# Kernel tuning notes

Measured on AMD Instinct MI355X. Metric: run time of the kernel, lower is better.

## Reference

```python
import jax, jax.numpy as jnp
import numpy as np

D_MODEL = 1024
NHEAD = 16
HEAD_DIM = D_MODEL // NHEAD
MAX_DIST = 128


def setup_inputs() -> dict:
    key = jax.random.key(0)
    ks = jax.random.split(key, 6)
    B, T = 2, 2048
    x = jax.random.normal(ks[0], (B, T, D_MODEL), dtype=jnp.float32)
    Wqkv = jax.random.normal(ks[1], (D_MODEL, 3 * D_MODEL), dtype=jnp.float32) * 0.02
    bqkv = jnp.zeros((3 * D_MODEL,), dtype=jnp.float32)
    Wout = jax.random.normal(ks[2], (D_MODEL, D_MODEL), dtype=jnp.float32) * 0.02
    bout = jnp.zeros((D_MODEL,), dtype=jnp.float32)
    rel_emb = jax.random.normal(ks[3], (2 * MAX_DIST + 1, NHEAD), dtype=jnp.float32) * 0.02
    return {"x": x, "Wqkv": Wqkv, "bqkv": bqkv, "Wout": Wout, "bout": bout, "rel_emb": rel_emb}


def _rel_bias(rel_emb, seq_len):
    pos = jnp.arange(seq_len)
    rel = pos[None, :] - pos[:, None]                       # [S,S]
    rel = jnp.clip(rel, -MAX_DIST, MAX_DIST) + MAX_DIST
    bias = rel_emb[rel]                                     # [S,S,H]
    bias = jnp.transpose(bias, (2, 0, 1))                   # [H,S,S]
    causal_mask = jnp.triu(jnp.ones((seq_len, seq_len), dtype=bool), k=1)
    return jnp.where(causal_mask[None, :, :], -jnp.inf, bias)


def reference(x, Wqkv, bqkv, Wout, bout, rel_emb):
    B, T, C = x.shape
    qkv = x @ Wqkv + bqkv                                   # [B,T,3C]
    q, k, v = jnp.split(qkv, 3, axis=-1)

    def split_heads(t):
        return jnp.transpose(t.reshape(B, T, NHEAD, HEAD_DIM), (0, 2, 1, 3))  # [B,H,T,Dh]

    q, k, v = split_heads(q), split_heads(k), split_heads(v)
    scale = jnp.sqrt(jnp.float32(HEAD_DIM))
    attn = jnp.einsum('bhtd,bhsd->bhts', q, k) / scale      # [B,H,T,S]
    bias = _rel_bias(rel_emb, T)                            # [H,T,S] (causal -inf mask baked in)
    attn = attn + bias[None, :, :, :]
    attn = jax.nn.softmax(attn, axis=-1)
    out = jnp.einsum('bhts,bhsd->bhtd', attn, v)            # [B,H,T,Dh]
    out = jnp.transpose(out, (0, 2, 1, 3)).reshape(B, T, C)
    return out @ Wout + bout
```

## Files before the change

### kernel.cpp

```cpp
#include <hip/hip_runtime.h>
#include <hip/hip_bf16.h>

typedef __attribute__((ext_vector_type(8))) short s8v;
typedef __attribute__((ext_vector_type(4))) float f4v;

__device__ __forceinline__ ushort f2bf(float f) {
    union { float f; unsigned u; } cv; cv.f = f;
    unsigned u = cv.u;
    unsigned lsb = (u >> 16) & 1u;
    u += 0x7fffu + lsb;
    return (ushort)(u >> 16);
}

typedef __attribute__((address_space(1))) void gvoid;
typedef __attribute__((address_space(3))) void lvoid;
__device__ __forceinline__ void gl_lds16(const ushort* g, ushort* l) {
    __builtin_amdgcn_global_load_lds((gvoid*)g, (lvoid*)l, 16, 0, 0);
}

__global__ void cast_bf16_kernel(const float* __restrict__ in, ushort* __restrict__ out, int n4) {
    int i = blockIdx.x * blockDim.x + threadIdx.x;
    if (i >= n4) return;
    float4 v = reinterpret_cast<const float4*>(in)[i];
    ushort4 o;
    o.x = f2bf(v.x); o.y = f2bf(v.y); o.z = f2bf(v.z); o.w = f2bf(v.w);
    reinterpret_cast<ushort4*>(out)[i] = o;
}

__global__ void transpose_cast_kernel(const float* __restrict__ in, ushort* __restrict__ out,
                                      int R, int C) {
    __shared__ float tile[32][33];
    int c0 = blockIdx.x * 32, r0 = blockIdx.y * 32;
    int tx = threadIdx.x & 31, ty = threadIdx.x >> 5;
    #pragma unroll
    for (int i = 0; i < 32; i += 8)
        tile[ty + i][tx] = in[(size_t)(r0 + ty + i) * C + c0 + tx];
    __syncthreads();
    #pragma unroll
    for (int i = 0; i < 32; i += 8)
        out[(size_t)(c0 + ty + i) * R + r0 + tx] = f2bf(tile[tx][ty + i]);
}

__global__ __launch_bounds__(256) void vtrans_kernel(
    const ushort* __restrict__ qkv, ushort* __restrict__ vt_g, int T)
{
    __shared__ ushort tile[64][72];
    const int sb = blockIdx.x * 64, bh = blockIdx.y;
    const int b = bh >> 4, h = bh & 15;
    const int t = threadIdx.x;
    const int r0 = t >> 3, c0 = (t & 7) * 8;
    const ushort* vsrc = qkv + (size_t)b * T * 3072 + 2048 + h * 64;
    *(s8v*)&tile[r0][c0]      = *(const s8v*)(vsrc + (size_t)(sb + r0) * 3072 + c0);
    *(s8v*)&tile[32 + r0][c0] = *(const s8v*)(vsrc + (size_t)(sb + 32 + r0) * 3072 + c0);
    __syncthreads();
    ushort* vdst = vt_g + (size_t)bh * 64 * T;
    s8v o0, o1;
    #pragma unroll
    for (int j = 0; j < 8; j++) {
        o0[j] = (short)tile[c0 + j][r0];
        o1[j] = (short)tile[c0 + j][32 + r0];
    }
    *(s8v*)(vdst + (size_t)r0 * T + sb + c0)        = o0;
    *(s8v*)(vdst + (size_t)(32 + r0) * T + sb + c0) = o1;
}

template <bool OUT_BF16>
__global__ __launch_bounds__(256) void gemm_bt_kernel(
    const ushort* __restrict__ A, const ushort* __restrict__ Bt,
    const float* __restrict__ bias, void* __restrict__ Cout,
    int M, int N, int K)
{
    __shared__ ushort As[128][64];
    __shared__ ushort Bs[128][64];
    const int t = threadIdx.x;
    const int m0 = blockIdx.y * 128, n0 = blockIdx.x * 128;
    const int wave = t >> 6, lane = t & 63;
    const int lr = lane & 15, lg = lane >> 4;
    const int wm = (wave >> 1) * 64, wn = (wave & 1) * 64;
    const int lrow = lane >> 3;
    const int lcol = (lane & 7) * 8;

    f4v acc[4][4];
    #pragma unroll
    for (int i = 0; i < 4; i++)
        #pragma unroll
        for (int j = 0; j < 4; j++)
            acc[i][j] = (f4v){0.f, 0.f, 0.f, 0.f};

    for (int k0 = 0; k0 < K; k0 += 64) {
        __syncthreads();
        #pragma unroll
        for (int i = 0; i < 4; i++) {
            int j = wave * 4 + i;
            int row = j * 8 + lrow;
            gl_lds16(A  + (size_t)(m0 + row) * K + k0 + lcol, &As[j * 8][0]);
            gl_lds16(Bt + (size_t)(n0 + row) * K + k0 + lcol, &Bs[j * 8][0]);
        }
        __syncthreads();
        #pragma unroll
        for (int ks = 0; ks < 64; ks += 32) {
            s8v af[4], bfr[4];
            #pragma unroll
            for (int mb = 0; mb < 4; mb++)
                af[mb] = *reinterpret_cast<const s8v*>(&As[wm + mb * 16 + lr][ks + lg * 8]);
            #pragma unroll
            for (int nb = 0; nb < 4; nb++)
                bfr[nb] = *reinterpret_cast<const s8v*>(&Bs[wn + nb * 16 + lr][ks + lg * 8]);
            #pragma unroll
            for (int mb = 0; mb < 4; mb++)
                #pragma unroll
                for (int nb = 0; nb < 4; nb++)
                    acc[mb][nb] = __builtin_amdgcn_mfma_f32_16x16x32_bf16(af[mb], bfr[nb], acc[mb][nb], 0, 0, 0);
        }
    }

    #pragma unroll
    for (int mb = 0; mb < 4; mb++) {
        #pragma unroll
        for (int nb = 0; nb < 4; nb++) {
            int col = n0 + wn + nb * 16 + lr;
            float bv = bias[col];
            #pragma unroll
            for (int r = 0; r < 4; r++) {
                int row = m0 + wm + mb * 16 + lg * 4 + r;
                float val = acc[mb][nb][r] + bv;
                if (OUT_BF16)
                    reinterpret_cast<ushort*>(Cout)[(size_t)row * N + col] = f2bf(val);
                else
                    reinterpret_cast<float*>(Cout)[(size_t)row * N + col] = val;
            }
        }
    }
}

__device__ __forceinline__ void attn_tile_sw(
    const s8v qf0, const s8v qf1, int q_abs, int qb, int sb,
    int lr, int lg,
    const ushort (*Ks)[72], const ushort (*Vs)[72],
    ushort (*pT)[72],
    const float* rel_lds,
    float& m, float& l, f4v* oT)
{
    const float SC = 0.125f * 1.44269504f;
    f4v sacc[4];
    __builtin_amdgcn_s_setprio(1);
    #pragma unroll
    for (int cb = 0; cb < 4; cb++) {
        sacc[cb] = (f4v){0.f, 0.f, 0.f, 0.f};
        s8v kf0 = *(const s8v*)&Ks[cb * 16 + lr][lg * 8];
        s8v kf1 = *(const s8v*)&Ks[cb * 16 + lr][32 + lg * 8];
        sacc[cb] = __builtin_amdgcn_mfma_f32_16x16x32_bf16(kf0, qf0, sacc[cb], 0, 0, 0);
        sacc[cb] = __builtin_amdgcn_mfma_f32_16x16x32_bf16(kf1, qf1, sacc[cb], 0, 0, 0);
    }
    __builtin_amdgcn_s_setprio(0);

    if (sb + 192 <= qb) {
        float c = rel_lds[0];
        #pragma unroll
        for (int cb = 0; cb < 4; cb++)
            #pragma unroll
            for (int r = 0; r < 4; r++)
                sacc[cb][r] = sacc[cb][r] * SC + c;
    } else {
        #pragma unroll
        for (int cb = 0; cb < 4; cb++) {
            #pragma unroll
            for (int r = 0; r < 4; r++) {
                int s = sb + cb * 16 + lg * 4 + r;
                int rel = s - q_abs;
                rel = (rel < -128 ? -128 : (rel > 128 ? 128 : rel)) + 128;
                float val = sacc[cb][r] * SC + rel_lds[rel];
                if (s > q_abs) val = -3.0e38f;
                sacc[cb][r] = val;
            }
        }
    }

    float pm0 = fmaxf(fmaxf(sacc[0][0], sacc[0][1]), fmaxf(sacc[0][2], sacc[0][3]));
    float pm1 = fmaxf(fmaxf(sacc[1][0], sacc[1][1]), fmaxf(sacc[1][2], sacc[1][3]));
    float pm2 = fmaxf(fmaxf(sacc[2][0], sacc[2][1]), fmaxf(sacc[2][2], sacc[2][3]));
    float pm3 = fmaxf(fmaxf(sacc[3][0], sacc[3][1]), fmaxf(sacc[3][2], sacc[3][3]));
    float pm = fmaxf(fmaxf(pm0, pm1), fmaxf(pm2, pm3));
    pm = fmaxf(pm, __shfl_xor(pm, 16, 64));
    pm = fmaxf(pm, __shfl_xor(pm, 32, 64));

    if (__any(pm > m + 8.0f)) {
        float mnew = fmaxf(m, pm);
        float alpha = exp2f(m - mnew);
        l *= alpha;
        #pragma unroll
        for (int d = 0; d < 4; d++)
            #pragma unroll
            for (int r = 0; r < 4; r++)
                oT[d][r] *= alpha;
        m = mnew;
    }

    float sum = 0.f;
    #pragma unroll
    for (int cb = 0; cb < 4; cb++) {
        #pragma unroll
        for (int r = 0; r < 4; r++) {
            float p = exp2f(sacc[cb][r] - m);
            sacc[cb][r] = p;
            sum += p;
        }
    }
    sum += __shfl_xor(sum, 16, 64);
    sum += __shfl_xor(sum, 32, 64);
    l += sum;

    #pragma unroll
    for (int cb = 0; cb < 4; cb++) {
        unsigned lo = (unsigned)f2bf(sacc[cb][0]) | ((unsigned)f2bf(sacc[cb][1]) << 16);
        unsigned hi = (unsigned)f2bf(sacc[cb][2]) | ((unsigned)f2bf(sacc[cb][3]) << 16);
        *(unsigned long long*)&pT[lr][cb * 16 + lg * 4] =
            (unsigned long long)lo | ((unsigned long long)hi << 32);
    }

    __builtin_amdgcn_s_setprio(1);
    #pragma unroll
    for (int ch = 0; ch < 2; ch++) {
        s8v pf = *(const s8v*)&pT[lr][ch * 32 + lg * 8];
        #pragma unroll
        for (int d = 0; d < 4; d++) {
            s8v vf = *(const s8v*)&Vs[d * 16 + lr][ch * 32 + lg * 8];
            oT[d] = __builtin_amdgcn_mfma_f32_16x16x32_bf16(vf, pf, oT[d], 0, 0, 0);
        }
    }
    __builtin_amdgcn_s_setprio(0);
}

__device__ __forceinline__ void store_O(
    f4v* oT, float l, int lr, int lg, int lane, int wave,
    ushort (*pT)[72], int qb, size_t rowb, int h, ushort* __restrict__ attn_out)
{
    float inv = 1.0f / l;
    #pragma unroll
    for (int d = 0; d < 4; d++) {
        unsigned lo = (unsigned)f2bf(oT[d][0] * inv) | ((unsigned)f2bf(oT[d][1] * inv) << 16);
        unsigned hi = (unsigned)f2bf(oT[d][2] * inv) | ((unsigned)f2bf(oT[d][3] * inv) << 16);
        *(unsigned long long*)&pT[lr][d * 16 + lg * 4] =
            (unsigned long long)lo | ((unsigned long long)hi << 32);
    }
    int q_r = lane >> 2, part = lane & 3;
    s8v a = *(const s8v*)&pT[q_r][part * 16];
    s8v b = *(const s8v*)&pT[q_r][part * 16 + 8];
    ushort* dst = attn_out + (rowb + qb + wave * 16 + q_r) * 1024 + h * 64 + part * 16;
    *(s8v*)dst = a;
    *(s8v*)(dst + 8) = b;
}

__global__ __launch_bounds__(256, 2) void attn_kernel(
    const ushort* __restrict__ qkv, const ushort* __restrict__ vt_g,
    const float* __restrict__ rel_emb, ushort* __restrict__ attn_out, int T)
{
    __shared__ ushort Ks[64][72];
    __shared__ ushort Vs[64][72];
    __shared__ ushort p_lds[4][16][72];
    __shared__ float rel_lds[257];

    const int t = threadIdx.x;
    const int nQ = T / 64;
    const int lo = blockIdx.x;
    const int hi = nQ - 1 - lo;
    const int qbL = lo * 64, qbH = hi * 64;
    const int bh = blockIdx.y;
    const int b = bh >> 4, h = bh & 15;
    const size_t rowb = (size_t)b * T;

    for (int i = t; i < 257; i += 256) rel_lds[i] = rel_emb[i * 16 + h] * 1.44269504f;

    const int wave = t >> 6, lane = t & 63;
    const int lr = lane & 15, lg = lane >> 4;
    const int sr = t >> 3, sc = (t & 7) * 8;

    const ushort* kbase = qkv + rowb * 3072 + 1024 + h * 64;
    const ushort* vbase = vt_g + (size_t)bh * 64 * T;

    const int qaL = qbL + wave * 16 + lr;
    const int qaH = qbH + wave * 16 + lr;
    const ushort* qptrL = qkv + (rowb + qaL) * 3072 + h * 64;
    s8v qL0 = *(const s8v*)(qptrL + lg * 8);
    s8v qL1 = *(const s8v*)(qptrL + 32 + lg * 8);
    const ushort* qptrH = qkv + (rowb + qaH) * 3072 + h * 64;
    s8v qH0 = *(const s8v*)(qptrH + lg * 8);
    s8v qH1 = *(const s8v*)(qptrH + 32 + lg * 8);

    float mL = -3.0e38f, lL = 0.f, mH = -3.0e38f, lH = 0.f;
    f4v oL[4], oH[4];
    #pragma unroll
    for (int d = 0; d < 4; d++) { oL[d] = (f4v){0.f,0.f,0.f,0.f}; oH[d] = (f4v){0.f,0.f,0.f,0.f}; }

    const int nt = hi + 1;

    s8v ka0 = *(const s8v*)(kbase + (size_t)sr * 3072 + sc);
    s8v ka1 = *(const s8v*)(kbase + (size_t)(32 + sr) * 3072 + sc);
    s8v va0 = *(const s8v*)(vbase + (size_t)sr * T + sc);
    s8v va1 = *(const s8v*)(vbase + (size_t)(32 + sr) * T + sc);

    for (int st = 0; st < nt; ++st) {
        const int sb = st * 64;
        __syncthreads();
        *(s8v*)&Ks[sr][sc]      = ka0;
        *(s8v*)&Ks[32 + sr][sc] = ka1;
        *(s8v*)&Vs[sr][sc]      = va0;
        *(s8v*)&Vs[32 + sr][sc] = va1;
        __syncthreads();

        if (st + 1 < nt) {
            const int sn = sb + 64;
            ka0 = *(const s8v*)(kbase + (size_t)(sn + sr) * 3072 + sc);
            ka1 = *(const s8v*)(kbase + (size_t)(sn + 32 + sr) * 3072 + sc);
            va0 = *(const s8v*)(vbase + (size_t)sr * T + sn + sc);
            va1 = *(const s8v*)(vbase + (size_t)(32 + sr) * T + sn + sc);
        }

        attn_tile_sw(qH0, qH1, qaH, qbH, sb, lr, lg, Ks, Vs, p_lds[wave], rel_lds, mH, lH, oH);
        if (st <= lo)
            attn_tile_sw(qL0, qL1, qaL, qbL, sb, lr, lg, Ks, Vs, p_lds[wave], rel_lds, mL, lL, oL);
    }

    store_O(oH, lH, lr, lg, lane, wave, p_lds[wave], qbH, rowb, h, attn_out);
    store_O(oL, lL, lr, lg, lane, wave, p_lds[wave], qbL, rowb, h, attn_out);
}

extern "C" void kernel_launch(void* const* d_in, const int* in_sizes, int n_in,
                              void* d_out, int out_size, void* d_ws, size_t ws_size,
                              hipStream_t stream) {
    const float* x       = (const float*)d_in[0];
    const float* Wqkv    = (const float*)d_in[1];
    const float* bqkv    = (const float*)d_in[2];
    const float* Wout    = (const float*)d_in[3];
    const float* bout    = (const float*)d_in[4];
    const float* rel_emb = (const float*)d_in[5];
    float* out = (float*)d_out;

    const int M = in_sizes[0] / 1024;
    const int T = 2048;
    const int B = M / T;

    ushort* x_bf = (ushort*)d_ws;
    ushort* Wq_t = x_bf + (size_t)M * 1024;
    ushort* Wo_t = Wq_t + (size_t)3072 * 1024;
    ushort* qkv  = Wo_t + (size_t)1024 * 1024;
    ushort* attn = qkv + (size_t)M * 3072;
    ushort* vt_g = attn + (size_t)M * 1024;

    hipLaunchKernelGGL(cast_bf16_kernel, dim3((M * 1024 / 4 + 255) / 256), dim3(256), 0, stream,
                       x, x_bf, M * 1024 / 4);
    hipLaunchKernelGGL(transpose_cast_kernel, dim3(3072 / 32, 1024 / 32), dim3(256), 0, stream,
                       Wqkv, Wq_t, 1024, 3072);
    hipLaunchKernelGGL(transpose_cast_kernel, dim3(1024 / 32, 1024 / 32), dim3(256), 0, stream,
                       Wout, Wo_t, 1024, 1024);
    hipLaunchKernelGGL((gemm_bt_kernel<true>), dim3(3072 / 128, M / 128), dim3(256), 0, stream,
                       x_bf, Wq_t, bqkv, (void*)qkv, M, 3072, 1024);
    hipLaunchKernelGGL(vtrans_kernel, dim3(T / 64, B * 16), dim3(256), 0, stream,
                       qkv, vt_g, T);
    hipLaunchKernelGGL(attn_kernel, dim3((T / 64) / 2, B * 16), dim3(256), 0, stream,
                       qkv, vt_g, rel_emb, attn, T);
    hipLaunchKernelGGL((gemm_bt_kernel<false>), dim3(1024 / 128, M / 128), dim3(256), 0, stream,
                       attn, Wo_t, bout, (void*)out, M, 1024, 1024);
}
```

Baseline: 225.2 us.

## Split attention work per wave across paired 32-row query tiles with rotated pairing

Each block now covers two 32-row query tiles, one low and one high, and assigns two waves to each, instead of every wave handling 16 rows from both a low and a high 64-row tile. Each wave holds only one set of accumulators, which lowers register pressure and allows launch bounds of 4 blocks per SM. The pairing index is rotated by the batch-head index to spread block durations. Waves on the low tile sit idle while the block streams the remaining key tiles for the high tile, and because the grid dimension is now the fixed constant 32, the kernel assumes T = 2048.

```diff
diff --git a/kernel.cpp b/kernel.cpp
--- a/kernel.cpp
+++ b/kernel.cpp
@@ -232,8 +232,8 @@
 }
 
 __device__ __forceinline__ void store_O(
-    f4v* oT, float l, int lr, int lg, int lane, int wave,
-    ushort (*pT)[72], int qb, size_t rowb, int h, ushort* __restrict__ attn_out)
+    f4v* oT, float l, int lr, int lg, int lane, int qrow0,
+    ushort (*pT)[72], size_t rowb, int h, ushort* __restrict__ attn_out)
 {
     float inv = 1.0f / l;
     #pragma unroll
@@ -246,12 +246,12 @@
     int q_r = lane >> 2, part = lane & 3;
     s8v a = *(const s8v*)&pT[q_r][part * 16];
     s8v b = *(const s8v*)&pT[q_r][part * 16 + 8];
-    ushort* dst = attn_out + (rowb + qb + wave * 16 + q_r) * 1024 + h * 64 + part * 16;
+    ushort* dst = attn_out + (rowb + qrow0 + q_r) * 1024 + h * 64 + part * 16;
     *(s8v*)dst = a;
     *(s8v*)(dst + 8) = b;
 }
 
-__global__ __launch_bounds__(256, 2) void attn_kernel(
+__global__ __launch_bounds__(256, 4) void attn_kernel(
     const ushort* __restrict__ qkv, const ushort* __restrict__ vt_g,
     const float* __restrict__ rel_emb, ushort* __restrict__ attn_out, int T)
 {
@@ -261,11 +261,9 @@
     __shared__ float rel_lds[257];
 
     const int t = threadIdx.x;
-    const int nQ = T / 64;
-    const int lo = blockIdx.x;
-    const int hi = nQ - 1 - lo;
-    const int qbL = lo * 64, qbH = hi * 64;
     const int bh = blockIdx.y;
+    const int p = (blockIdx.x + bh) & 31;
+    const int lo = p, hi = 63 - p;
     const int b = bh >> 4, h = bh & 15;
     const size_t rowb = (size_t)b * T;
 
@@ -275,31 +273,31 @@
     const int lr = lane & 15, lg = lane >> 4;
     const int sr = t >> 3, sc = (t & 7) * 8;
 
+    const int my_tile = (wave < 2) ? hi : lo;
+    const int qtb = my_tile * 32;
+    const int qrow0 = qtb + (wave & 1) * 16;
+    const int qa = qrow0 + lr;
+    const int my_nt = (qtb + 31) / 64 + 1;
+    const int ntH = ((63 - p) * 32 + 31) / 64 + 1;
+
     const ushort* kbase = qkv + rowb * 3072 + 1024 + h * 64;
     const ushort* vbase = vt_g + (size_t)bh * 64 * T;
 
-    const int qaL = qbL + wave * 16 + lr;
-    const int qaH = qbH + wave * 16 + lr;
-    const ushort* qptrL = qkv + (rowb + qaL) * 3072 + h * 64;
-    s8v qL0 = *(const s8v*)(qptrL + lg * 8);
-    s8v qL1 = *(const s8v*)(qptrL + 32 + lg * 8);
-    const ushort* qptrH = qkv + (rowb + qaH) * 3072 + h * 64;
-    s8v qH0 = *(const s8v*)(qptrH + lg * 8);
-    s8v qH1 = *(const s8v*)(qptrH + 32 + lg * 8);
-
-    float mL = -3.0e38f, lL = 0.f, mH = -3.0e38f, lH = 0.f;
-    f4v oL[4], oH[4];
-    #pragma unroll
-    for (int d = 0; d < 4; d++) { oL[d] = (f4v){0.f,0.f,0.f,0.f}; oH[d] = (f4v){0.f,0.f,0.f,0.f}; }
-
-    const int nt = hi + 1;
+    const ushort* qptr = qkv + (rowb + qa) * 3072 + h * 64;
+    s8v qf0 = *(const s8v*)(qptr + lg * 8);
+    s8v qf1 = *(const s8v*)(qptr + 32 + lg * 8);
+
+    float m = -3.0e38f, l = 0.f;
+    f4v oT[4];
+    #pragma unroll
+    for (int d = 0; d < 4; d++) oT[d] = (f4v){0.f, 0.f, 0.f, 0.f};
 
     s8v ka0 = *(const s8v*)(kbase + (size_t)sr * 3072 + sc);
     s8v ka1 = *(const s8v*)(kbase + (size_t)(32 + sr) * 3072 + sc);
     s8v va0 = *(const s8v*)(vbase + (size_t)sr * T + sc);
     s8v va1 = *(const s8v*)(vbase + (size_t)(32 + sr) * T + sc);
 
-    for (int st = 0; st < nt; ++st) {
+    for (int st = 0; st < ntH; ++st) {
         const int sb = st * 64;
         __syncthreads();
         *(s8v*)&Ks[sr][sc]      = ka0;
@@ -308,7 +306,7 @@
         *(s8v*)&Vs[32 + sr][sc] = va1;
         __syncthreads();
 
-        if (st + 1 < nt) {
+        if (st + 1 < ntH) {
             const int sn = sb + 64;
             ka0 = *(const s8v*)(kbase + (size_t)(sn + sr) * 3072 + sc);
             ka1 = *(const s8v*)(kbase + (size_t)(sn + 32 + sr) * 3072 + sc);
@@ -316,13 +314,11 @@
             va1 = *(const s8v*)(vbase + (size_t)(32 + sr) * T + sn + sc);
         }
 
-        attn_tile_sw(qH0, qH1, qaH, qbH, sb, lr, lg, Ks, Vs, p_lds[wave], rel_lds, mH, lH, oH);
-        if (st <= lo)
-            attn_tile_sw(qL0, qL1, qaL, qbL, sb, lr, lg, Ks, Vs, p_lds[wave], rel_lds, mL, lL, oL);
-    }
-
-    store_O(oH, lH, lr, lg, lane, wave, p_lds[wave], qbH, rowb, h, attn_out);
-    store_O(oL, lL, lr, lg, lane, wave, p_lds[wave], qbL, rowb, h, attn_out);
+        if (st < my_nt)
+            attn_tile_sw(qf0, qf1, qa, qtb, sb, lr, lg, Ks, Vs, p_lds[wave], rel_lds, m, l, oT);
+    }
+
+    store_O(oT, l, lr, lg, lane, qrow0, p_lds[wave], rowb, h, attn_out);
 }
 
 extern "C" void kernel_launch(void* const* d_in, const int* in_sizes, int n_in,
@@ -357,7 +353,7 @@
                        x_bf, Wq_t, bqkv, (void*)qkv, M, 3072, 1024);
     hipLaunchKernelGGL(vtrans_kernel, dim3(T / 64, B * 16), dim3(256), 0, stream,
                        qkv, vt_g, T);
-    hipLaunchKernelGGL(attn_kernel, dim3((T / 64) / 2, B * 16), dim3(256), 0, stream,
+    hipLaunchKernelGGL(attn_kernel, dim3(32, B * 16), dim3(256), 0, stream,
                        qkv, vt_g, rel_emb, attn, T);
     hipLaunchKernelGGL((gemm_bt_kernel<false>), dim3(1024 / 128, M / 128), dim3(256), 0, stream,
                        attn, Wo_t, bout, (void*)out, M, 1024, 1024);
```

After: 234.4 us. 4.1% more time.
